# Optimization experiments

Hardware: AMD Instinct MI355X
Metric: run time of the kernel (lower is better)

The kernel has to match this reference:

```python
import jax, jax.numpy as jnp
import numpy as np
from jax import lax

B, T_IN, T_OUT = 32, 384, 400
N_MEL, ENC, ATT_RNN, DEC_RNN, PRENET, ATT_DIM = 80, 512, 1024, 1024, 256, 128
LOC_F, LOC_K = 32, 31
NEG = -1e9  # stand-in for -inf score_mask_value (safe for softmax grad)


def setup_inputs() -> dict:
    key = jax.random.key(0)
    ks = jax.random.split(key, 20)
    g = lambda i, shape, s=0.02: jax.random.normal(ks[i], shape, dtype=jnp.float32) * s
    return {
        "memory": jax.random.normal(ks[0], (B, T_IN, ENC), dtype=jnp.float32),
        "decoder_inputs": jax.random.normal(ks[1], (B, N_MEL, T_OUT), dtype=jnp.float32),
        "memory_lengths": jax.random.randint(ks[2], (B,), T_IN // 2, T_IN + 1, dtype=jnp.int32),
        "prenet_w1": g(3, (PRENET, N_MEL)),
        "prenet_w2": g(4, (PRENET, PRENET)),
        "att_rnn_wih": g(5, (4 * ATT_RNN, PRENET + ENC)),
        "att_rnn_whh": g(6, (4 * ATT_RNN, ATT_RNN)),
        "att_rnn_bih": jnp.zeros((4 * ATT_RNN,), jnp.float32),
        "att_rnn_bhh": jnp.zeros((4 * ATT_RNN,), jnp.float32),
        "query_w": g(7, (ATT_DIM, ATT_RNN)),
        "memory_w": g(8, (ATT_DIM, ENC)),
        "v_w": g(9, (1, ATT_DIM)),
        "loc_conv_w": g(10, (LOC_F, 2, LOC_K)),
        "loc_dense_w": g(11, (ATT_DIM, LOC_F)),
        "dec_rnn_wih": g(12, (4 * DEC_RNN, ATT_RNN + ENC)),
        "dec_rnn_whh": g(13, (4 * DEC_RNN, DEC_RNN)),
        "dec_rnn_bih": jnp.zeros((4 * DEC_RNN,), jnp.float32),
        "dec_rnn_bhh": jnp.zeros((4 * DEC_RNN,), jnp.float32),
        "proj_w": g(14, (N_MEL, DEC_RNN + ENC)),
        "proj_b": jnp.zeros((N_MEL,), jnp.float32),
        "gate_w": g(15, (1, DEC_RNN + ENC)),
        "gate_b": jnp.zeros((1,), jnp.float32),
    }


def _lstm_cell(x, h, c, wih, whh, bih, bhh):
    gates = x @ wih.T + bih + h @ whh.T + bhh
    i, f, g, o = jnp.split(gates, 4, axis=-1)
    c2 = jax.nn.sigmoid(f) * c + jax.nn.sigmoid(i) * jnp.tanh(g)
    return jax.nn.sigmoid(o) * jnp.tanh(c2), c2


def reference(memory, decoder_inputs, memory_lengths, prenet_w1, prenet_w2,
              att_rnn_wih, att_rnn_whh, att_rnn_bih, att_rnn_bhh,
              query_w, memory_w, v_w, loc_conv_w, loc_dense_w,
              dec_rnn_wih, dec_rnn_whh, dec_rnn_bih, dec_rnn_bhh,
              proj_w, proj_b, gate_w, gate_b):
    pad = (LOC_K - 1) // 2
    pad_mask = jnp.arange(T_IN)[None, :] >= memory_lengths[:, None]  # (B, T_in), True = padded
    processed_memory = jnp.einsum('bte,ae->bta', memory, memory_w)  # (B, T_in, A)

    # parse_decoder_inputs + go frame: (T_out+1, B, n_mel)
    dec_in = jnp.concatenate([jnp.zeros((1, B, N_MEL), memory.dtype),
                              jnp.transpose(decoder_inputs, (2, 0, 1))], axis=0)
    # Prenet on whole teacher-forced sequence (eval: no dropout)
    pre = jax.nn.relu(jnp.einsum('tbm,pm->tbp', dec_in, prenet_w1))
    pre = jax.nn.relu(jnp.einsum('tbp,qp->tbq', pre, prenet_w2))  # (T_out+1, B, prenet)
    xs = pre[:-1]  # T_out decode steps

    def step(carry, x):
        ah, ac, dh, dc, aw, awc, ctx = carry
        # attention RNN
        ah, ac = _lstm_cell(jnp.concatenate([x, ctx], -1), ah, ac,
                            att_rnn_wih, att_rnn_whh, att_rnn_bih, att_rnn_bhh)
        # location-sensitive additive attention
        pq = (ah @ query_w.T)[:, None, :]  # (B, 1, A)
        cat = jnp.stack([aw, awc], axis=1)  # (B, 2, T_in)
        loc = lax.conv_general_dilated(cat, loc_conv_w, (1,), [(pad, pad)],
                                       dimension_numbers=('NCH', 'OIH', 'NCH'))  # (B, F, T_in)
        ploc = jnp.einsum('bft,af->bta', loc, loc_dense_w)  # (B, T_in, A)
        e = jnp.squeeze(jnp.tanh(pq + ploc + processed_memory) @ v_w.T, -1)  # (B, T_in)
        e = jnp.where(pad_mask, NEG, e)
        w = jax.nn.softmax(e, axis=1)
        ctx = jnp.einsum('bt,bte->be', w, memory)  # (B, enc)
        awc = awc + w
        # decoder RNN
        dh, dc = _lstm_cell(jnp.concatenate([ah, ctx], -1), dh, dc,
                            dec_rnn_wih, dec_rnn_whh, dec_rnn_bih, dec_rnn_bhh)
        hc = jnp.concatenate([dh, ctx], -1)  # (B, dec+enc)
        mel = hc @ proj_w.T + proj_b  # (B, n_mel)
        gate = hc @ gate_w.T + gate_b  # (B, 1)
        return (ah, ac, dh, dc, w, awc, ctx), (mel, gate, w)

    z = lambda d: jnp.zeros((B, d), memory.dtype)
    carry0 = (z(ATT_RNN), z(ATT_RNN), z(DEC_RNN), z(DEC_RNN),
              jnp.zeros((B, T_IN), memory.dtype), jnp.zeros((B, T_IN), memory.dtype), z(ENC))
    _, (mels, gates, aligns) = lax.scan(step, carry0, xs)
    mel_outputs = jnp.transpose(mels, (1, 2, 0))  # (B, n_mel, T_out)
    gate_outputs = jnp.transpose(jnp.squeeze(gates, -1), (1, 0))  # (B, T_out)
    alignments = jnp.transpose(aligns, (1, 0, 2))  # (B, T_out, T_in)
    return mel_outputs, gate_outputs, alignments
```

## Files before the change

### kernel.cpp

```cpp
#include <hip/hip_runtime.h>

typedef _Float16 h16;
typedef _Float16 half8 __attribute__((ext_vector_type(8)));
typedef float f32x4 __attribute__((ext_vector_type(4)));

#define NEGV -1000000000.0f
#define MFMA16(a,b,c) __builtin_amdgcn_mfma_f32_16x16x32_f16(a,b,c,0,0,0)

struct Params {
  const float *memory, *dec_in; const int *memlen;
  const float *w1, *w2;
  const float *awih, *awhh, *abih, *abhh;
  const float *qw, *mw, *vw, *lcw, *ldw;
  const float *dwih, *dwhh, *dbih, *dbhh;
  const float *pw, *pb, *gw, *gb;
  float *out, *ws;
};

constexpr long long XALLF_H = 0;
constexpr long long PMH_H   = 3276800;
constexpr long long PLB_H   = 4849664;
constexpr long long AWIHF_H = 6422528;
constexpr long long AWHHF_H = 9568256;
constexpr long long DWIHF_H = 13762560;
constexpr long long DWHHF_H = 20054016;
constexpr long long LCWF_H  = 24248320;
constexpr long long LDWF_H  = 24250368;
constexpr long long AHF_H   = 24254464;
constexpr long long DHF_H   = 24320000;
constexpr long long CTXF_H  = 24352768;
constexpr long long MEMF_H  = 24812544;
constexpr long long PWF_H   = 31104000;
constexpr long long ZERO_F0 = 12127232;
constexpr long long AC_F    = 12184576;
constexpr long long DC_F    = 12217344;
constexpr long long AW_F    = 12250112;
constexpr long long AWC_F   = 12262400;
constexpr long long DPART_F = 12274688;
constexpr long long BAR_F   = 12405760;
constexpr int  ZERO_LEN = 278528;
constexpr unsigned NBLK = 512;
constexpr long long GATE0  = 1024000;
constexpr long long ALIGN0 = 1036800;

union SMem {
  float pmstage[12][512];
  struct { float x[5][80]; float l1[5][256]; } pre;
  struct { float red[8][2][16][17]; } g;
  struct { float awseg[2][128]; h16 im2[96][72]; h16 locT[96][32];
           unsigned p16[96][64]; } ploc;
  struct { float ah[1024]; float pq[128]; float pqp[4][128]; float vv[128];
           float e[384]; float w[384]; float red[16];
           float ctxred[2][256][2]; } row;
  struct { float hc[1536]; float mp[80][4]; float gacc; } mel;
};

__device__ __forceinline__ float sigf(float x){ return 1.0f/(1.0f+__expf(-x)); }
__device__ __forceinline__ float tanhfast(float x){ float e2 = __expf(2.0f*x); return 1.0f - 2.0f/(e2+1.0f); }

__device__ __forceinline__ float aldf(const float* p){
  return __hip_atomic_load(p, __ATOMIC_RELAXED, __HIP_MEMORY_SCOPE_AGENT);
}
__device__ __forceinline__ void astf(float* p, float v){
  __hip_atomic_store(p, v, __ATOMIC_RELAXED, __HIP_MEMORY_SCOPE_AGENT);
}
__device__ __forceinline__ unsigned long long aldu64(const h16* p){
  return __hip_atomic_load((const unsigned long long*)p, __ATOMIC_RELAXED, __HIP_MEMORY_SCOPE_AGENT);
}
__device__ __forceinline__ half8 ald16(const h16* p){
  union { unsigned long long q[2]; half8 v; } u;
  u.q[0] = __hip_atomic_load((const unsigned long long*)p,     __ATOMIC_RELAXED, __HIP_MEMORY_SCOPE_AGENT);
  u.q[1] = __hip_atomic_load(((const unsigned long long*)p)+1, __ATOMIC_RELAXED, __HIP_MEMORY_SCOPE_AGENT);
  return u.v;
}
__device__ __forceinline__ void asth(h16* p, float v){
  union { h16 h; unsigned short s; } u; u.h = (h16)v;
  __hip_atomic_store((unsigned short*)p, u.s, __ATOMIC_RELAXED, __HIP_MEMORY_SCOPE_AGENT);
}
__device__ __forceinline__ void astu32(unsigned* p, unsigned v){
  __hip_atomic_store(p, v, __ATOMIC_RELAXED, __HIP_MEMORY_SCOPE_AGENT);
}

__device__ __forceinline__ void gbar(unsigned* cnts, unsigned ep, bool full){
  __syncthreads();
  if (threadIdx.x == 0){
    if (full) __threadfence();
    __hip_atomic_fetch_add(&cnts[(blockIdx.x & 7)*64], 1u, __ATOMIC_RELEASE, __HIP_MEMORY_SCOPE_AGENT);
    const unsigned tgt = ep*NBLK;
    for (;;){
      unsigned s = 0;
      #pragma unroll
      for (int i = 0; i < 8; ++i)
        s += __hip_atomic_load(&cnts[i*64], __ATOMIC_RELAXED, __HIP_MEMORY_SCOPE_AGENT);
      if (s >= tgt) break;
      __builtin_amdgcn_s_sleep(4);
    }
    if (full) __threadfence();
  }
  __syncthreads();
}

__global__ void init_kernel(float* ws){
  unsigned* c = (unsigned*)(ws + BAR_F);
  if (threadIdx.x < 512) c[threadIdx.x] = 0u;
}

__global__ __launch_bounds__(512, 4)
void decoder_kernel(Params P){
  __shared__ SMem sm;
  const int tid = threadIdx.x;
  const int bid = blockIdx.x;
  float* ws = P.ws;
  h16*   wsh = (h16*)ws;
  unsigned* bar = (unsigned*)(ws + BAR_F);
  unsigned ep = 0;

  const int lane = tid & 63, wv = tid >> 6;
  const int i16 = lane & 15, q = lane >> 4;

  {
    const long long gtid = (long long)bid*512 + tid;
    const long long GS = 262144;
    for (long long i = gtid; i < ZERO_LEN; i += GS) ws[ZERO_F0 + i] = 0.f;
    for (long long i = gtid; i < 3145728; i += GS) wsh[AWIHF_H+i] = (h16)P.awih[i];
    for (long long i = gtid; i < 4194304; i += GS) wsh[AWHHF_H+i] = (h16)P.awhh[i];
    for (long long i = gtid; i < 6291456; i += GS) wsh[DWIHF_H+i] = (h16)P.dwih[i];
    for (long long i = gtid; i < 4194304; i += GS) wsh[DWHHF_H+i] = (h16)P.dwhh[i];
    for (long long i = gtid; i < 6291456; i += GS) wsh[MEMF_H+i] = (h16)P.memory[i];
    for (long long i = gtid; i < 122880; i += GS) wsh[PWF_H+i] = (h16)P.pw[i];
    for (long long i = gtid; i < 2048; i += GS){
      int f = (int)(i >> 6), kk = (int)(i & 63), ch = kk >> 5, k = kk & 31;
      wsh[LCWF_H+i] = (k < 31) ? (h16)P.lcw[f*62 + ch*31 + k] : (h16)0.f;
    }
    for (long long i = gtid; i < 4096; i += GS) wsh[LDWF_H+i] = (h16)P.ldw[i];
  }
  {
    const int b = bid >> 4, part = bid & 15;
    for (int sub = 0; sub < 2; ++sub){
      const int t0 = part*24 + sub*12;
      __syncthreads();
      for (int i = tid; i < 1536; i += 512){
        int row = i >> 7, c4 = (i & 127) << 2;
        *reinterpret_cast<float4*>(&sm.pmstage[row][c4]) =
          *reinterpret_cast<const float4*>(P.memory + ((long long)(b*384 + t0 + row))*512 + c4);
      }
      __syncthreads();
      const int a = tid & 127, th = tid >> 7;
      float acc[3] = {0,0,0};
      const float* mwr = P.mw + (long long)a*512;
      for (int e = 0; e < 512; ++e){
        float wvv = mwr[e];
        #pragma unroll
        for (int jj = 0; jj < 3; ++jj) acc[jj] += wvv*sm.pmstage[th*3+jj][e];
      }
      #pragma unroll
      for (int jj = 0; jj < 3; ++jj)
        wsh[PMH_H + ((long long)b*128 + a)*384 + t0 + th*3 + jj] = (h16)acc[jj];
    }
  }
  {
    for (int batch = 0; batch < 5; ++batch){
      const int pbase = bid*25 + batch*5;
      __syncthreads();
      for (int i = tid; i < 400; i += 512){
        int j = i/80, m = i%80;
        int p = pbase + j; int tq = p >> 5, bb = p & 31;
        float v = 0.f;
        if (tq > 0) v = P.dec_in[((long long)bb*80 + m)*400 + (tq-1)];
        sm.pre.x[j][m] = v;
      }
      __syncthreads();
      {
        float acc[5] = {0,0,0,0,0};
        if (tid < 256){
          const float* w1r = P.w1 + (long long)tid*80;
          for (int m = 0; m < 80; ++m){
            float wvv = w1r[m];
            #pragma unroll
            for (int j = 0; j < 5; ++j) acc[j] += wvv*sm.pre.x[j][m];
          }
        }
        __syncthreads();
        if (tid < 256){
          #pragma unroll
          for (int j = 0; j < 5; ++j) sm.pre.l1[j][tid] = fmaxf(acc[j], 0.f);
        }
      }
      __syncthreads();
      if (tid < 256){
        float acc[5] = {0,0,0,0,0};
        const float* w2r = P.w2 + (long long)tid*256;
        for (int pp = 0; pp < 256; ++pp){
          float wvv = w2r[pp];
          #pragma unroll
          for (int j = 0; j < 5; ++j) acc[j] += wvv*sm.pre.l1[j][pp];
        }
        #pragma unroll
        for (int j = 0; j < 5; ++j){
          int p = pbase + j; int tq = p >> 5, bb = p & 31;
          wsh[XALLF_H + ((long long)tq*32 + bb)*256 + tid] = (h16)fmaxf(acc[j], 0.f);
        }
      }
    }
  }
  gbar(bar, ++ep, true);

  for (int t = 0; t <= 400; ++t){
    const int cur = t & 1, prv = (t+1) & 1;

    if (bid < 256){
      if (t < 400){
        const int u0 = bid*4;
        const int n = ((i16 >> 2)*1024) + u0 + (i16 & 3);
        f32x4 acc0 = {0,0,0,0}, acc1 = {0,0,0,0};
        const long long prvO = (long long)prv*32768;
        for (int s = wv*7; s < wv*7 + 7; ++s){
          const int k0 = s*32;
          const h16* pA = (k0 < 768) ? wsh + AWIHF_H + (long long)n*768 + k0 + q*8
                                     : wsh + AWHHF_H + (long long)n*1024 + (k0-768) + q*8;
          half8 A = *(const half8*)pA;
          half8 B0, B1;
          if (k0 < 256){
            B0 = *(const half8*)(wsh + XALLF_H + ((long long)t*32 + i16)*256 + k0 + q*8);
            B1 = *(const half8*)(wsh + XALLF_H + ((long long)t*32 + 16 + i16)*256 + k0 + q*8);
          } else if (k0 < 768){
            B0 = ald16(wsh + CTXF_H + i16*512 + (k0-256) + q*8);
            B1 = ald16(wsh + CTXF_H + (16+i16)*512 + (k0-256) + q*8);
          } else {
            B0 = ald16(wsh + AHF_H + prvO + i16*1024 + (k0-768) + q*8);
            B1 = ald16(wsh + AHF_H + prvO + (16+i16)*1024 + (k0-768) + q*8);
          }
          acc0 = MFMA16(A, B0, acc0);
          acc1 = MFMA16(A, B1, acc1);
        }
        #pragma unroll
        for (int r = 0; r < 4; ++r){
          sm.g.red[wv][0][q*4+r][i16] = acc0[r];
          sm.g.red[wv][1][q*4+r][i16] = acc1[r];
        }
        __syncthreads();
        if (tid < 128){
          const int uu = tid >> 5, b = tid & 31;
          const int bt = b >> 4, c = b & 15;
          float g4[4];
          #pragma unroll
          for (int g = 0; g < 4; ++g){
            const int tr = g*4 + uu;
            float v = 0.f;
            #pragma unroll
            for (int w8 = 0; w8 < 8; ++w8) v += sm.g.red[w8][bt][tr][c];
            const int ng = g*1024 + u0 + uu;
            g4[g] = v + P.abih[ng] + P.abhh[ng];
          }
          const long long idx = (long long)b*1024 + u0 + uu;
          float c2 = sigf(g4[1])*ws[AC_F + idx] + sigf(g4[0])*tanhfast(g4[2]);
          ws[AC_F + idx] = c2;
          asth(wsh + AHF_H + (long long)cur*32768 + idx, sigf(g4[3])*tanhfast(c2));
        }
      }
    } else if (bid < 384){
      if (t < 400){
        const int pb = bid - 256, b = pb >> 2, tbase = (pb & 3)*96;
        for (int i = tid; i < 252; i += 512){
          int ch = i / 126, ix = i % 126;
          int pos = tbase - 15 + ix;
          float v = 0.f;
          if (pos >= 0 && pos < 384)
            v = aldf(ws + (ch ? AWC_F : AW_F) + b*384 + pos);
          sm.ploc.awseg[ch][ix] = v;
        }
        __syncthreads();
        for (int i = tid; i < 96*64; i += 512){
          int tt = i >> 6, kk = i & 63, ch = kk >> 5, k = kk & 31;
          sm.ploc.im2[tt][kk] = (k < 31) ? (h16)sm.ploc.awseg[ch][tt + k] : (h16)0.f;
        }
        __syncthreads();
        #pragma unroll
        for (int p = 0; p < 2; ++p){
          int tile = wv + p*8;
          if (tile < 12){
            int tT = tile % 6, tF = tile / 6;
            f32x4 a = {0,0,0,0};
            #pragma unroll
            for (int ks = 0; ks < 2; ++ks){
              half8 A = *(const half8*)&sm.ploc.im2[tT*16 + i16][ks*32 + q*8];
              half8 B = *(const half8*)(wsh + LCWF_H + (tF*16 + i16)*64 + ks*32 + q*8);
              a = MFMA16(A, B, a);
            }
            #pragma unroll
            for (int r = 0; r < 4; ++r)
              sm.ploc.locT[tT*16 + q*4 + r][tF*16 + i16] = (h16)a[r];
          }
        }
        __syncthreads();
        unsigned short* s16 = (unsigned short*)&sm.ploc.p16[0][0];
        #pragma unroll
        for (int p = 0; p < 6; ++p){
          int tile = wv + p*8;
          int tT = tile % 6, tA = tile / 6;
          half8 A = *(const half8*)&sm.ploc.locT[tT*16 + i16][q*8];
          half8 B = *(const half8*)(wsh + LDWF_H + (tA*16 + i16)*32 + q*8);
          f32x4 a = {0,0,0,0};
          a = MFMA16(A, B, a);
          int aa = tA*16 + i16;
          union { unsigned long long u; h16 h[4]; } pmu;
          pmu.u = *(const unsigned long long*)
              (wsh + PMH_H + ((long long)b*128 + aa)*384 + tbase + tT*16 + q*4);
          #pragma unroll
          for (int r = 0; r < 4; ++r){
            union { h16 h; unsigned short s; } cv;
            cv.h = (h16)(a[r] + (float)pmu.h[r]);
            s16[(tT*16 + q*4 + r)*128 + aa] = cv.s;
          }
        }
        __syncthreads();
        unsigned* plbu = (unsigned*)(wsh + PLB_H);
        for (int i = tid; i < 96*64; i += 512){
          int tt = i >> 6, a2 = i & 63;
          astu32(plbu + ((long long)b*384 + tbase + tt)*64 + a2, sm.ploc.p16[tt][a2]);
        }
      }
    } else {
      if (t >= 1){
        const int u0 = (bid-384)*8;
        const int jt = wv & 1, kh = wv >> 1;
        const int n = ((i16 >> 2)*1024) + u0 + jt*4 + (i16 & 3);
        f32x4 acc0 = {0,0,0,0}, acc1 = {0,0,0,0};
        for (int s = kh*4; s < kh*4 + 4; ++s){
          const int k0 = s*32;
          half8 A = *(const half8*)(wsh + DWIHF_H + (long long)n*1536 + 1024 + k0 + q*8);
          half8 B0 = ald16(wsh + CTXF_H + i16*512 + k0 + q*8);
          half8 B1 = ald16(wsh + CTXF_H + (16+i16)*512 + k0 + q*8);
          acc0 = MFMA16(A, B0, acc0);
          acc1 = MFMA16(A, B1, acc1);
        }
        #pragma unroll
        for (int r = 0; r < 4; ++r){
          sm.g.red[wv][0][q*4+r][i16] = acc0[r];
          sm.g.red[wv][1][q*4+r][i16] = acc1[r];
        }
        __syncthreads();
        if (tid < 256){
          const int uu8 = tid >> 5, b = tid & 31;
          const int j2 = uu8 >> 2, uu = uu8 & 3;
          const int bt = b >> 4, c = b & 15;
          const int unit = u0 + j2*4 + uu;
          float g4[4];
          #pragma unroll
          for (int g = 0; g < 4; ++g){
            const int tr = g*4 + uu;
            const int ng = g*1024 + unit;
            float v = sm.g.red[j2][bt][tr][c]   + sm.g.red[j2+2][bt][tr][c]
                    + sm.g.red[j2+4][bt][tr][c] + sm.g.red[j2+6][bt][tr][c];
            g4[g] = v + aldf(ws + DPART_F + (long long)b*4096 + ng)
                  + P.dbih[ng] + P.dbhh[ng];
          }
          const long long idx = (long long)b*1024 + unit;
          float c2 = sigf(g4[1])*ws[DC_F + idx] + sigf(g4[0])*tanhfast(g4[2]);
          ws[DC_F + idx] = c2;
          asth(wsh + DHF_H + idx, sigf(g4[3])*tanhfast(c2));
        }
      }
    }
    gbar(bar, ++ep, false);

    if (bid < 32){
      if (t < 400){
        const int b = bid;
        const int len = P.memlen[b];
        if (tid < 256){
          union { unsigned long long u; h16 h[4]; } hu;
          hu.u = aldu64(wsh + AHF_H + (long long)cur*32768 + b*1024 + tid*4);
          #pragma unroll
          for (int j = 0; j < 4; ++j) sm.row.ah[tid*4+j] = (float)hu.h[j];
        }
        if (tid < 128) sm.row.vv[tid] = P.vw[tid];
        __syncthreads();
        {
          const int a = tid & 127, kh4 = tid >> 7;
          const float* qr  = P.qw + (long long)a*1024 + kh4*256;
          const float* ahs = &sm.row.ah[kh4*256];
          float acc = 0.f;
          for (int k = 0; k < 256; k += 4){
            float4 wq = *reinterpret_cast<const float4*>(qr + k);
            acc += wq.x*ahs[k] + wq.y*ahs[k+1] + wq.z*ahs[k+2] + wq.w*ahs[k+3];
          }
          sm.row.pqp[kh4][a] = acc;
        }
        __syncthreads();
        if (tid < 128) sm.row.pq[tid] = sm.row.pqp[0][tid] + sm.row.pqp[1][tid]
                                      + sm.row.pqp[2][tid] + sm.row.pqp[3][tid];
        __syncthreads();
        {
          const int tt = tid;
          if (tt < 384){
            float acc;
            if (tt < len){
              acc = 0.f;
              const unsigned long long* plp = (const unsigned long long*)
                  (wsh + PLB_H + ((long long)b*384 + tt)*128);
              for (int a0 = 0; a0 < 32; ++a0){
                union { unsigned long long u; h16 h[4]; } hu;
                hu.u = __hip_atomic_load(plp + a0, __ATOMIC_RELAXED, __HIP_MEMORY_SCOPE_AGENT);
                #pragma unroll
                for (int j = 0; j < 4; ++j)
                  acc += sm.row.vv[a0*4+j]*tanhfast(sm.row.pq[a0*4+j] + (float)hu.h[j]);
              }
            } else acc = NEGV;
            sm.row.e[tt] = acc;
          }
        }
        __syncthreads();
        float m = NEGV;
        for (int tt = tid; tt < 384; tt += 512) m = fmaxf(m, sm.row.e[tt]);
        for (int o = 32; o; o >>= 1) m = fmaxf(m, __shfl_xor(m, o, 64));
        if ((tid & 63) == 0) sm.row.red[tid >> 6] = m;
        __syncthreads();
        float mx = sm.row.red[0];
        #pragma unroll
        for (int w8 = 1; w8 < 8; ++w8) mx = fmaxf(mx, sm.row.red[w8]);
        float s = 0.f;
        for (int tt = tid; tt < 384; tt += 512){
          float wvv = (tt < len) ? __expf(sm.row.e[tt] - mx) : 0.f;
          sm.row.w[tt] = wvv; s += wvv;
        }
        for (int o = 32; o; o >>= 1) s += __shfl_xor(s, o, 64);
        if ((tid & 63) == 0) sm.row.red[8 + (tid >> 6)] = s;
        __syncthreads();
        float ssum = sm.row.red[8];
        #pragma unroll
        for (int w8 = 1; w8 < 8; ++w8) ssum += sm.row.red[8+w8];
        const float inv = 1.f/ssum;
        for (int tt = tid; tt < 384; tt += 512){
          float wvv = sm.row.w[tt]*inv;
          sm.row.w[tt] = wvv;
          astf(ws + AW_F + b*384 + tt, wvv);
          float oldc = aldf(ws + AWC_F + b*384 + tt);
          astf(ws + AWC_F + b*384 + tt, oldc + wvv);
          P.out[ALIGN0 + ((long long)b*400 + t)*384 + tt] = wvv;
        }
        __syncthreads();
        {
          const int col = tid & 255, rg = tid >> 8;
          const unsigned* mrow = (const unsigned*)(wsh + MEMF_H) + (long long)b*98304;
          float acc0 = 0.f, acc1 = 0.f;
          for (int t4 = rg*48; t4 < rg*48 + 48; ++t4){
            float4 w4 = *reinterpret_cast<const float4*>(&sm.row.w[t4*4]);
            const unsigned* m0 = mrow + t4*1024 + col;
            unsigned v0 = m0[0], v1 = m0[256], v2 = m0[512], v3 = m0[768];
            union { unsigned u; h16 h[2]; } d0, d1, d2, d3;
            d0.u = v0; d1.u = v1; d2.u = v2; d3.u = v3;
            acc0 += w4.x*(float)d0.h[0] + w4.y*(float)d1.h[0]
                  + w4.z*(float)d2.h[0] + w4.w*(float)d3.h[0];
            acc1 += w4.x*(float)d0.h[1] + w4.y*(float)d1.h[1]
                  + w4.z*(float)d2.h[1] + w4.w*(float)d3.h[1];
          }
          sm.row.ctxred[rg][col][0] = acc0;
          sm.row.ctxred[rg][col][1] = acc1;
          __syncthreads();
          if (tid < 256){
            union { h16 h[2]; unsigned u; } cv;
            cv.h[0] = (h16)(sm.row.ctxred[0][tid][0] + sm.row.ctxred[1][tid][0]);
            cv.h[1] = (h16)(sm.row.ctxred[0][tid][1] + sm.row.ctxred[1][tid][1]);
            astu32((unsigned*)(wsh + CTXF_H) + b*256 + tid, cv.u);
          }
        }
      }
    } else if (bid < 288){
      if (t < 400){
        const int n0 = (bid-32)*16;
        const int n = n0 + i16;
        f32x4 acc0 = {0,0,0,0}, acc1 = {0,0,0,0};
        const long long curO = (long long)cur*32768;
        for (int s = wv*8; s < wv*8 + 8; ++s){
          const int k0 = s*32;
          const h16* pA = (k0 < 1024) ? wsh + DWIHF_H + (long long)n*1536 + k0 + q*8
                                      : wsh + DWHHF_H + (long long)n*1024 + (k0-1024) + q*8;
          half8 A = *(const half8*)pA;
          half8 B0, B1;
          if (k0 < 1024){
            B0 = ald16(wsh + AHF_H + curO + i16*1024 + k0 + q*8);
            B1 = ald16(wsh + AHF_H + curO + (16+i16)*1024 + k0 + q*8);
          } else {
            B0 = ald16(wsh + DHF_H + i16*1024 + (k0-1024) + q*8);
            B1 = ald16(wsh + DHF_H + (16+i16)*1024 + (k0-1024) + q*8);
          }
          acc0 = MFMA16(A, B0, acc0);
          acc1 = MFMA16(A, B1, acc1);
        }
        #pragma unroll
        for (int r = 0; r < 4; ++r){
          sm.g.red[wv][0][q*4+r][i16] = acc0[r];
          sm.g.red[wv][1][q*4+r][i16] = acc1[r];
        }
        __syncthreads();
        if (tid < 256){
          const int r16 = tid & 15, c = tid >> 4;
          #pragma unroll
          for (int bt = 0; bt < 2; ++bt){
            float v = 0.f;
            #pragma unroll
            for (int w8 = 0; w8 < 8; ++w8) v += sm.g.red[w8][bt][r16][c];
            astf(ws + DPART_F + (long long)(bt*16 + c)*4096 + n0 + r16, v);
          }
        }
      }
    } else if (bid < 320){
      if (t >= 1){
        const int b = bid - 288;
        for (int i = tid; i < 384; i += 512){
          union { unsigned long long u; h16 h[4]; } hu;
          hu.u = (i < 256) ? aldu64(wsh + DHF_H + b*1024 + i*4)
                           : aldu64(wsh + CTXF_H + b*512 + (i-256)*4);
          #pragma unroll
          for (int j = 0; j < 4; ++j) sm.mel.hc[i*4+j] = (float)hu.h[j];
        }
        __syncthreads();
        if (tid < 320){
          const int r = tid >> 2, h4 = tid & 3;
          const h16* pr = wsh + PWF_H + (long long)r*1536 + h4*384;
          const float* hcp = &sm.mel.hc[h4*384];
          float acc = 0.f;
          for (int k = 0; k < 384; k += 8){
            half8 wq = *(const half8*)(pr + k);
            acc += (float)wq[0]*hcp[k]   + (float)wq[1]*hcp[k+1]
                 + (float)wq[2]*hcp[k+2] + (float)wq[3]*hcp[k+3]
                 + (float)wq[4]*hcp[k+4] + (float)wq[5]*hcp[k+5]
                 + (float)wq[6]*hcp[k+6] + (float)wq[7]*hcp[k+7];
          }
          sm.mel.mp[r][h4] = acc;
        } else if (tid >= 384 && tid < 448){
          const int l = tid - 384;
          const float* gp  = P.gw + l*24;
          const float* hcp = &sm.mel.hc[l*24];
          float acc = 0.f;
          #pragma unroll
          for (int k = 0; k < 24; ++k) acc += gp[k]*hcp[k];
          for (int o = 32; o; o >>= 1) acc += __shfl_xor(acc, o, 64);
          if (l == 0) sm.mel.gacc = acc;
        }
        __syncthreads();
        if (tid < 80)
          P.out[((long long)b*80 + tid)*400 + (t-1)] =
            sm.mel.mp[tid][0] + sm.mel.mp[tid][1] + sm.mel.mp[tid][2] + sm.mel.mp[tid][3] + P.pb[tid];
        if (tid == 80)
          P.out[GATE0 + (long long)b*400 + (t-1)] = sm.mel.gacc + P.gb[0];
      }
    }
    gbar(bar, ++ep, false);
  }
}

extern "C" void kernel_launch(void* const* d_in, const int* in_sizes, int n_in,
                              void* d_out, int out_size, void* d_ws, size_t ws_size,
                              hipStream_t stream) {
  (void)in_sizes; (void)n_in; (void)out_size; (void)ws_size;
  Params p;
  p.memory = (const float*)d_in[0];
  p.dec_in = (const float*)d_in[1];
  p.memlen = (const int*)d_in[2];
  p.w1   = (const float*)d_in[3];
  p.w2   = (const float*)d_in[4];
  p.awih = (const float*)d_in[5];
  p.awhh = (const float*)d_in[6];
  p.abih = (const float*)d_in[7];
  p.abhh = (const float*)d_in[8];
  p.qw   = (const float*)d_in[9];
  p.mw   = (const float*)d_in[10];
  p.vw   = (const float*)d_in[11];
  p.lcw  = (const float*)d_in[12];
  p.ldw  = (const float*)d_in[13];
  p.dwih = (const float*)d_in[14];
  p.dwhh = (const float*)d_in[15];
  p.dbih = (const float*)d_in[16];
  p.dbhh = (const float*)d_in[17];
  p.pw   = (const float*)d_in[18];
  p.pb   = (const float*)d_in[19];
  p.gw   = (const float*)d_in[20];
  p.gb   = (const float*)d_in[21];
  p.out  = (float*)d_out;
  p.ws   = (float*)d_ws;

  hipLaunchKernelGGL(init_kernel, dim3(1), dim3(512), 0, stream, p.ws);
  hipLaunchKernelGGL(decoder_kernel, dim3(512), dim3(512), 0, stream, p);
}
```

Before: 43.81 ms.

## Double block size to 1024 threads and split per-step work across more waves

Launches the persistent decoder with 1024-thread blocks and reassigns work so each wave computes one batch half of the MFMA gate GEMMs instead of two, halves the K-range per wave in the decoder context GEMM, and splits the query, context and mel-projection reductions into more partial sums. It also pre-converts query_w to fp16 in the workspace so the query projection reads half the bytes. The intent is to shorten the per-step critical path in this latency-bound recurrent loop by exposing more parallel waves per block. It risks heavier register pressure under launch_bounds(1024, 8), and the grid-wide barrier now waits on twice as many threads per block, which may not co-reside.

```diff
diff --git a/kernel.cpp b/kernel.cpp
--- a/kernel.cpp
+++ b/kernel.cpp
@@ -31,6 +31,7 @@
 constexpr long long CTXF_H  = 24352768;
 constexpr long long MEMF_H  = 24812544;
 constexpr long long PWF_H   = 31104000;
+constexpr long long QWF_H   = 31226880;
 constexpr long long ZERO_F0 = 12127232;
 constexpr long long AC_F    = 12184576;
 constexpr long long DC_F    = 12217344;
@@ -46,13 +47,13 @@
 union SMem {
   float pmstage[12][512];
   struct { float x[5][80]; float l1[5][256]; } pre;
-  struct { float red[8][2][16][17]; } g;
+  struct { float red[16][2][16][17]; } g;
   struct { float awseg[2][128]; h16 im2[96][72]; h16 locT[96][32];
            unsigned p16[96][64]; } ploc;
-  struct { float ah[1024]; float pq[128]; float pqp[4][128]; float vv[128];
-           float e[384]; float w[384]; float red[16];
-           float ctxred[2][256][2]; } row;
-  struct { float hc[1536]; float mp[80][4]; float gacc; } mel;
+  struct { float ah[1024]; float pq[128]; float pqp[8][128]; float vv[128];
+           float e[384]; float w[384]; float red[32];
+           float ctxred[4][256][2]; } row;
+  struct { float hc[1536]; float mp[80][8]; float gacc; } mel;
 };
 
 __device__ __forceinline__ float sigf(float x){ return 1.0f/(1.0f+__expf(-x)); }
@@ -105,7 +106,7 @@
   if (threadIdx.x < 512) c[threadIdx.x] = 0u;
 }
 
-__global__ __launch_bounds__(512, 4)
+__global__ __launch_bounds__(1024, 8)
 void decoder_kernel(Params P){
   __shared__ SMem sm;
   const int tid = threadIdx.x;
@@ -119,8 +120,8 @@
   const int i16 = lane & 15, q = lane >> 4;
 
   {
-    const long long gtid = (long long)bid*512 + tid;
-    const long long GS = 262144;
+    const long long gtid = (long long)bid*1024 + tid;
+    const long long GS = 524288;
     for (long long i = gtid; i < ZERO_LEN; i += GS) ws[ZERO_F0 + i] = 0.f;
     for (long long i = gtid; i < 3145728; i += GS) wsh[AWIHF_H+i] = (h16)P.awih[i];
     for (long long i = gtid; i < 4194304; i += GS) wsh[AWHHF_H+i] = (h16)P.awhh[i];
@@ -128,6 +129,7 @@
     for (long long i = gtid; i < 4194304; i += GS) wsh[DWHHF_H+i] = (h16)P.dwhh[i];
     for (long long i = gtid; i < 6291456; i += GS) wsh[MEMF_H+i] = (h16)P.memory[i];
     for (long long i = gtid; i < 122880; i += GS) wsh[PWF_H+i] = (h16)P.pw[i];
+    for (long long i = gtid; i < 131072; i += GS) wsh[QWF_H+i] = (h16)P.qw[i];
     for (long long i = gtid; i < 2048; i += GS){
       int f = (int)(i >> 6), kk = (int)(i & 63), ch = kk >> 5, k = kk & 31;
       wsh[LCWF_H+i] = (k < 31) ? (h16)P.lcw[f*62 + ch*31 + k] : (h16)0.f;
@@ -139,30 +141,32 @@
     for (int sub = 0; sub < 2; ++sub){
       const int t0 = part*24 + sub*12;
       __syncthreads();
-      for (int i = tid; i < 1536; i += 512){
+      for (int i = tid; i < 1536; i += 1024){
         int row = i >> 7, c4 = (i & 127) << 2;
         *reinterpret_cast<float4*>(&sm.pmstage[row][c4]) =
           *reinterpret_cast<const float4*>(P.memory + ((long long)(b*384 + t0 + row))*512 + c4);
       }
       __syncthreads();
-      const int a = tid & 127, th = tid >> 7;
-      float acc[3] = {0,0,0};
-      const float* mwr = P.mw + (long long)a*512;
-      for (int e = 0; e < 512; ++e){
-        float wvv = mwr[e];
-        #pragma unroll
-        for (int jj = 0; jj < 3; ++jj) acc[jj] += wvv*sm.pmstage[th*3+jj][e];
-      }
-      #pragma unroll
-      for (int jj = 0; jj < 3; ++jj)
-        wsh[PMH_H + ((long long)b*128 + a)*384 + t0 + th*3 + jj] = (h16)acc[jj];
+      if (tid < 512){
+        const int a = tid & 127, th = tid >> 7;
+        float acc[3] = {0,0,0};
+        const float* mwr = P.mw + (long long)a*512;
+        for (int e = 0; e < 512; ++e){
+          float wvv = mwr[e];
+          #pragma unroll
+          for (int jj = 0; jj < 3; ++jj) acc[jj] += wvv*sm.pmstage[th*3+jj][e];
+        }
+        #pragma unroll
+        for (int jj = 0; jj < 3; ++jj)
+          wsh[PMH_H + ((long long)b*128 + a)*384 + t0 + th*3 + jj] = (h16)acc[jj];
+      }
     }
   }
   {
     for (int batch = 0; batch < 5; ++batch){
       const int pbase = bid*25 + batch*5;
       __syncthreads();
-      for (int i = tid; i < 400; i += 512){
+      for (int i = tid; i < 400; i += 1024){
         int j = i/80, m = i%80;
         int p = pbase + j; int tq = p >> 5, bb = p & 31;
         float v = 0.f;
@@ -211,44 +215,35 @@
     if (bid < 256){
       if (t < 400){
         const int u0 = bid*4;
+        const int w8 = wv & 7, bt = wv >> 3;
         const int n = ((i16 >> 2)*1024) + u0 + (i16 & 3);
-        f32x4 acc0 = {0,0,0,0}, acc1 = {0,0,0,0};
+        const int row0 = bt*16 + i16;
+        f32x4 acc = {0,0,0,0};
         const long long prvO = (long long)prv*32768;
-        for (int s = wv*7; s < wv*7 + 7; ++s){
+        for (int s = w8*7; s < w8*7 + 7; ++s){
           const int k0 = s*32;
           const h16* pA = (k0 < 768) ? wsh + AWIHF_H + (long long)n*768 + k0 + q*8
                                      : wsh + AWHHF_H + (long long)n*1024 + (k0-768) + q*8;
           half8 A = *(const half8*)pA;
-          half8 B0, B1;
-          if (k0 < 256){
-            B0 = *(const half8*)(wsh + XALLF_H + ((long long)t*32 + i16)*256 + k0 + q*8);
-            B1 = *(const half8*)(wsh + XALLF_H + ((long long)t*32 + 16 + i16)*256 + k0 + q*8);
-          } else if (k0 < 768){
-            B0 = ald16(wsh + CTXF_H + i16*512 + (k0-256) + q*8);
-            B1 = ald16(wsh + CTXF_H + (16+i16)*512 + (k0-256) + q*8);
-          } else {
-            B0 = ald16(wsh + AHF_H + prvO + i16*1024 + (k0-768) + q*8);
-            B1 = ald16(wsh + AHF_H + prvO + (16+i16)*1024 + (k0-768) + q*8);
-          }
-          acc0 = MFMA16(A, B0, acc0);
-          acc1 = MFMA16(A, B1, acc1);
-        }
-        #pragma unroll
-        for (int r = 0; r < 4; ++r){
-          sm.g.red[wv][0][q*4+r][i16] = acc0[r];
-          sm.g.red[wv][1][q*4+r][i16] = acc1[r];
-        }
+          half8 B;
+          if (k0 < 256)      B = *(const half8*)(wsh + XALLF_H + ((long long)t*32 + row0)*256 + k0 + q*8);
+          else if (k0 < 768) B = ald16(wsh + CTXF_H + row0*512 + (k0-256) + q*8);
+          else               B = ald16(wsh + AHF_H + prvO + (long long)row0*1024 + (k0-768) + q*8);
+          acc = MFMA16(A, B, acc);
+        }
+        #pragma unroll
+        for (int r = 0; r < 4; ++r) sm.g.red[w8][bt][q*4+r][i16] = acc[r];
         __syncthreads();
         if (tid < 128){
           const int uu = tid >> 5, b = tid & 31;
-          const int bt = b >> 4, c = b & 15;
+          const int bt2 = b >> 4, c = b & 15;
           float g4[4];
           #pragma unroll
           for (int g = 0; g < 4; ++g){
             const int tr = g*4 + uu;
             float v = 0.f;
             #pragma unroll
-            for (int w8 = 0; w8 < 8; ++w8) v += sm.g.red[w8][bt][tr][c];
+            for (int w = 0; w < 8; ++w) v += sm.g.red[w][bt2][tr][c];
             const int ng = g*1024 + u0 + uu;
             g4[g] = v + P.abih[ng] + P.abhh[ng];
           }
@@ -261,7 +256,7 @@
     } else if (bid < 384){
       if (t < 400){
         const int pb = bid - 256, b = pb >> 2, tbase = (pb & 3)*96;
-        for (int i = tid; i < 252; i += 512){
+        for (int i = tid; i < 252; i += 1024){
           int ch = i / 126, ix = i % 126;
           int pos = tbase - 15 + ix;
           float v = 0.f;
@@ -270,14 +265,13 @@
           sm.ploc.awseg[ch][ix] = v;
         }
         __syncthreads();
-        for (int i = tid; i < 96*64; i += 512){
+        for (int i = tid; i < 96*64; i += 1024){
           int tt = i >> 6, kk = i & 63, ch = kk >> 5, k = kk & 31;
           sm.ploc.im2[tt][kk] = (k < 31) ? (h16)sm.ploc.awseg[ch][tt + k] : (h16)0.f;
         }
         __syncthreads();
-        #pragma unroll
-        for (int p = 0; p < 2; ++p){
-          int tile = wv + p*8;
+        {
+          int tile = wv;
           if (tile < 12){
             int tT = tile % 6, tF = tile / 6;
             f32x4 a = {0,0,0,0};
@@ -295,8 +289,8 @@
         __syncthreads();
         unsigned short* s16 = (unsigned short*)&sm.ploc.p16[0][0];
         #pragma unroll
-        for (int p = 0; p < 6; ++p){
-          int tile = wv + p*8;
+        for (int p = 0; p < 3; ++p){
+          int tile = wv + p*16;
           int tT = tile % 6, tA = tile / 6;
           half8 A = *(const half8*)&sm.ploc.locT[tT*16 + i16][q*8];
           half8 B = *(const half8*)(wsh + LDWF_H + (tA*16 + i16)*32 + q*8);
@@ -315,7 +309,7 @@
         }
         __syncthreads();
         unsigned* plbu = (unsigned*)(wsh + PLB_H);
-        for (int i = tid; i < 96*64; i += 512){
+        for (int i = tid; i < 96*64; i += 1024){
           int tt = i >> 6, a2 = i & 63;
           astu32(plbu + ((long long)b*384 + tbase + tt)*64 + a2, sm.ploc.p16[tt][a2]);
         }
@@ -326,7 +320,7 @@
         const int jt = wv & 1, kh = wv >> 1;
         const int n = ((i16 >> 2)*1024) + u0 + jt*4 + (i16 & 3);
         f32x4 acc0 = {0,0,0,0}, acc1 = {0,0,0,0};
-        for (int s = kh*4; s < kh*4 + 4; ++s){
+        for (int s = kh*2; s < kh*2 + 2; ++s){
           const int k0 = s*32;
           half8 A = *(const half8*)(wsh + DWIHF_H + (long long)n*1536 + 1024 + k0 + q*8);
           half8 B0 = ald16(wsh + CTXF_H + i16*512 + k0 + q*8);
@@ -350,8 +344,9 @@
           for (int g = 0; g < 4; ++g){
             const int tr = g*4 + uu;
             const int ng = g*1024 + unit;
-            float v = sm.g.red[j2][bt][tr][c]   + sm.g.red[j2+2][bt][tr][c]
-                    + sm.g.red[j2+4][bt][tr][c] + sm.g.red[j2+6][bt][tr][c];
+            float v = 0.f;
+            #pragma unroll
+            for (int k = 0; k < 8; ++k) v += sm.g.red[j2 + 2*k][bt][tr][c];
             g4[g] = v + aldf(ws + DPART_F + (long long)b*4096 + ng)
                   + P.dbih[ng] + P.dbhh[ng];
           }
@@ -377,19 +372,26 @@
         if (tid < 128) sm.row.vv[tid] = P.vw[tid];
         __syncthreads();
         {
-          const int a = tid & 127, kh4 = tid >> 7;
-          const float* qr  = P.qw + (long long)a*1024 + kh4*256;
-          const float* ahs = &sm.row.ah[kh4*256];
+          const int a = tid & 127, kh8 = tid >> 7;
+          const h16* qr = wsh + QWF_H + (long long)a*1024 + kh8*128;
+          const float* ahs = &sm.row.ah[kh8*128];
           float acc = 0.f;
-          for (int k = 0; k < 256; k += 4){
-            float4 wq = *reinterpret_cast<const float4*>(qr + k);
-            acc += wq.x*ahs[k] + wq.y*ahs[k+1] + wq.z*ahs[k+2] + wq.w*ahs[k+3];
-          }
-          sm.row.pqp[kh4][a] = acc;
-        }
-        __syncthreads();
-        if (tid < 128) sm.row.pq[tid] = sm.row.pqp[0][tid] + sm.row.pqp[1][tid]
-                                      + sm.row.pqp[2][tid] + sm.row.pqp[3][tid];
+          for (int k = 0; k < 128; k += 8){
+            half8 wq = *(const half8*)(qr + k);
+            acc += (float)wq[0]*ahs[k]   + (float)wq[1]*ahs[k+1]
+                 + (float)wq[2]*ahs[k+2] + (float)wq[3]*ahs[k+3]
+                 + (float)wq[4]*ahs[k+4] + (float)wq[5]*ahs[k+5]
+                 + (float)wq[6]*ahs[k+6] + (float)wq[7]*ahs[k+7];
+          }
+          sm.row.pqp[kh8][a] = acc;
+        }
+        __syncthreads();
+        if (tid < 128){
+          float pqv = 0.f;
+          #pragma unroll
+          for (int k = 0; k < 8; ++k) pqv += sm.row.pqp[k][tid];
+          sm.row.pq[tid] = pqv;
+        }
         __syncthreads();
         {
           const int tt = tid;
@@ -412,26 +414,26 @@
         }
         __syncthreads();
         float m = NEGV;
-        for (int tt = tid; tt < 384; tt += 512) m = fmaxf(m, sm.row.e[tt]);
+        for (int tt = tid; tt < 384; tt += 1024) m = fmaxf(m, sm.row.e[tt]);
         for (int o = 32; o; o >>= 1) m = fmaxf(m, __shfl_xor(m, o, 64));
         if ((tid & 63) == 0) sm.row.red[tid >> 6] = m;
         __syncthreads();
         float mx = sm.row.red[0];
         #pragma unroll
-        for (int w8 = 1; w8 < 8; ++w8) mx = fmaxf(mx, sm.row.red[w8]);
+        for (int w = 1; w < 16; ++w) mx = fmaxf(mx, sm.row.red[w]);
         float s = 0.f;
-        for (int tt = tid; tt < 384; tt += 512){
+        for (int tt = tid; tt < 384; tt += 1024){
           float wvv = (tt < len) ? __expf(sm.row.e[tt] - mx) : 0.f;
           sm.row.w[tt] = wvv; s += wvv;
         }
         for (int o = 32; o; o >>= 1) s += __shfl_xor(s, o, 64);
-        if ((tid & 63) == 0) sm.row.red[8 + (tid >> 6)] = s;
-        __syncthreads();
-        float ssum = sm.row.red[8];
-        #pragma unroll
-        for (int w8 = 1; w8 < 8; ++w8) ssum += sm.row.red[8+w8];
+        if ((tid & 63) == 0) sm.row.red[16 + (tid >> 6)] = s;
+        __syncthreads();
+        float ssum = sm.row.red[16];
+        #pragma unroll
+        for (int w = 1; w < 16; ++w) ssum += sm.row.red[16+w];
         const float inv = 1.f/ssum;
-        for (int tt = tid; tt < 384; tt += 512){
+        for (int tt = tid; tt < 384; tt += 1024){
           float wvv = sm.row.w[tt]*inv;
           sm.row.w[tt] = wvv;
           astf(ws + AW_F + b*384 + tt, wvv);
@@ -444,7 +446,7 @@
           const int col = tid & 255, rg = tid >> 8;
           const unsigned* mrow = (const unsigned*)(wsh + MEMF_H) + (long long)b*98304;
           float acc0 = 0.f, acc1 = 0.f;
-          for (int t4 = rg*48; t4 < rg*48 + 48; ++t4){
+          for (int t4 = rg*24; t4 < rg*24 + 24; ++t4){
             float4 w4 = *reinterpret_cast<const float4*>(&sm.row.w[t4*4]);
             const unsigned* m0 = mrow + t4*1024 + col;
             unsigned v0 = m0[0], v1 = m0[256], v2 = m0[512], v3 = m0[768];
@@ -460,8 +462,10 @@
           __syncthreads();
           if (tid < 256){
             union { h16 h[2]; unsigned u; } cv;
-            cv.h[0] = (h16)(sm.row.ctxred[0][tid][0] + sm.row.ctxred[1][tid][0]);
-            cv.h[1] = (h16)(sm.row.ctxred[0][tid][1] + sm.row.ctxred[1][tid][1]);
+            cv.h[0] = (h16)(sm.row.ctxred[0][tid][0] + sm.row.ctxred[1][tid][0]
+                          + sm.row.ctxred[2][tid][0] + sm.row.ctxred[3][tid][0]);
+            cv.h[1] = (h16)(sm.row.ctxred[0][tid][1] + sm.row.ctxred[1][tid][1]
+                          + sm.row.ctxred[2][tid][1] + sm.row.ctxred[3][tid][1]);
             astu32((unsigned*)(wsh + CTXF_H) + b*256 + tid, cv.u);
           }
         }
@@ -470,45 +474,38 @@
       if (t < 400){
         const int n0 = (bid-32)*16;
         const int n = n0 + i16;
-        f32x4 acc0 = {0,0,0,0}, acc1 = {0,0,0,0};
+        const int w8 = wv & 7, bt = wv >> 3;
+        const int row0 = bt*16 + i16;
+        f32x4 acc = {0,0,0,0};
         const long long curO = (long long)cur*32768;
-        for (int s = wv*8; s < wv*8 + 8; ++s){
+        for (int s = w8*8; s < w8*8 + 8; ++s){
           const int k0 = s*32;
           const h16* pA = (k0 < 1024) ? wsh + DWIHF_H + (long long)n*1536 + k0 + q*8
                                       : wsh + DWHHF_H + (long long)n*1024 + (k0-1024) + q*8;
           half8 A = *(const half8*)pA;
-          half8 B0, B1;
-          if (k0 < 1024){
-            B0 = ald16(wsh + AHF_H + curO + i16*1024 + k0 + q*8);
-            B1 = ald16(wsh + AHF_H + curO + (16+i16)*1024 + k0 + q*8);
-          } else {
-            B0 = ald16(wsh + DHF_H + i16*1024 + (k0-1024) + q*8);
-            B1 = ald16(wsh + DHF_H + (16+i16)*1024 + (k0-1024) + q*8);
-          }
-          acc0 = MFMA16(A, B0, acc0);
-          acc1 = MFMA16(A, B1, acc1);
-        }
-        #pragma unroll
-        for (int r = 0; r < 4; ++r){
-          sm.g.red[wv][0][q*4+r][i16] = acc0[r];
-          sm.g.red[wv][1][q*4+r][i16] = acc1[r];
-        }
+          half8 B;
+          if (k0 < 1024) B = ald16(wsh + AHF_H + curO + (long long)row0*1024 + k0 + q*8);
+          else           B = ald16(wsh + DHF_H + (long long)row0*1024 + (k0-1024) + q*8);
+          acc = MFMA16(A, B, acc);
+        }
+        #pragma unroll
+        for (int r = 0; r < 4; ++r) sm.g.red[w8][bt][q*4+r][i16] = acc[r];
         __syncthreads();
         if (tid < 256){
           const int r16 = tid & 15, c = tid >> 4;
           #pragma unroll
-          for (int bt = 0; bt < 2; ++bt){
+          for (int bt2 = 0; bt2 < 2; ++bt2){
             float v = 0.f;
             #pragma unroll
-            for (int w8 = 0; w8 < 8; ++w8) v += sm.g.red[w8][bt][r16][c];
-            astf(ws + DPART_F + (long long)(bt*16 + c)*4096 + n0 + r16, v);
+            for (int w = 0; w < 8; ++w) v += sm.g.red[w][bt2][r16][c];
+            astf(ws + DPART_F + (long long)(bt2*16 + c)*4096 + n0 + r16, v);
           }
         }
       }
     } else if (bid < 320){
       if (t >= 1){
         const int b = bid - 288;
-        for (int i = tid; i < 384; i += 512){
+        for (int i = tid; i < 384; i += 1024){
           union { unsigned long long u; h16 h[4]; } hu;
           hu.u = (i < 256) ? aldu64(wsh + DHF_H + b*1024 + i*4)
                            : aldu64(wsh + CTXF_H + b*512 + (i-256)*4);
@@ -516,21 +513,21 @@
           for (int j = 0; j < 4; ++j) sm.mel.hc[i*4+j] = (float)hu.h[j];
         }
         __syncthreads();
-        if (tid < 320){
-          const int r = tid >> 2, h4 = tid & 3;
-          const h16* pr = wsh + PWF_H + (long long)r*1536 + h4*384;
-          const float* hcp = &sm.mel.hc[h4*384];
+        if (tid < 640){
+          const int r = tid >> 3, h8 = tid & 7;
+          const h16* pr = wsh + PWF_H + (long long)r*1536 + h8*192;
+          const float* hcp = &sm.mel.hc[h8*192];
           float acc = 0.f;
-          for (int k = 0; k < 384; k += 8){
+          for (int k = 0; k < 192; k += 8){
             half8 wq = *(const half8*)(pr + k);
             acc += (float)wq[0]*hcp[k]   + (float)wq[1]*hcp[k+1]
                  + (float)wq[2]*hcp[k+2] + (float)wq[3]*hcp[k+3]
                  + (float)wq[4]*hcp[k+4] + (float)wq[5]*hcp[k+5]
                  + (float)wq[6]*hcp[k+6] + (float)wq[7]*hcp[k+7];
           }
-          sm.mel.mp[r][h4] = acc;
-        } else if (tid >= 384 && tid < 448){
-          const int l = tid - 384;
+          sm.mel.mp[r][h8] = acc;
+        } else if (tid >= 768 && tid < 832){
+          const int l = tid - 768;
           const float* gp  = P.gw + l*24;
           const float* hcp = &sm.mel.hc[l*24];
           float acc = 0.f;
@@ -540,9 +537,12 @@
           if (l == 0) sm.mel.gacc = acc;
         }
         __syncthreads();
-        if (tid < 80)
-          P.out[((long long)b*80 + tid)*400 + (t-1)] =
-            sm.mel.mp[tid][0] + sm.mel.mp[tid][1] + sm.mel.mp[tid][2] + sm.mel.mp[tid][3] + P.pb[tid];
+        if (tid < 80){
+          float v = P.pb[tid];
+          #pragma unroll
+          for (int k = 0; k < 8; ++k) v += sm.mel.mp[tid][k];
+          P.out[((long long)b*80 + tid)*400 + (t-1)] = v;
+        }
         if (tid == 80)
           P.out[GATE0 + (long long)b*400 + (t-1)] = sm.mel.gacc + P.gb[0];
       }
@@ -582,5 +582,5 @@
   p.ws   = (float*)d_ws;
 
   hipLaunchKernelGGL(init_kernel, dim3(1), dim3(512), 0, stream, p.ws);
-  hipLaunchKernelGGL(decoder_kernel, dim3(512), dim3(512), 0, stream, p);
-}
+  hipLaunchKernelGGL(decoder_kernel, dim3(512), dim3(1024), 0, stream, p);
+}
```

Result: slower. 45.12 ms (+3.0%).
